# Optimization experiments

Measured on AMD Instinct MI355X. Metric: run time of the kernel, lower is better.

Reference implementation:

```python
import jax, jax.numpy as jnp
import numpy as np

B, N, L = 128, 100, 30
D_FEAT, C, CMD, T = 2112, 512, 512, 4
NEG = -1e30
INV_SQRT_C = np.float32(1.0 / np.sqrt(C))


def setup_inputs() -> dict:
    key = jax.random.key(0)
    ks = iter(jax.random.split(key, 64))

    def lin(out, inn):
        s = 1.0 / np.sqrt(inn)
        W = jax.random.uniform(next(ks), (out, inn), minval=-s, maxval=s, dtype=jnp.float32)
        b = jax.random.uniform(next(ks), (out,), minval=-s, maxval=s, dtype=jnp.float32)
        return W, b

    inp = {}
    inp['images'] = jax.random.normal(next(ks), (B, N, D_FEAT), dtype=jnp.float32)
    inp['q_encoding'] = jax.random.normal(next(ks), (B, CMD), dtype=jnp.float32)
    inp['lstm_outputs'] = jax.random.normal(next(ks), (B, L, CMD), dtype=jnp.float32)
    inp['W_initKB'], inp['b_initKB'] = lin(C, D_FEAT)
    inp['initMem'] = jax.random.normal(next(ks), (1, 1, C), dtype=jnp.float32)
    inp['W_qIn'], inp['b_qIn'] = lin(CMD, CMD)
    Ws, bs = zip(*[lin(CMD, CMD) for _ in range(T)])
    inp['W_qIn2'] = jnp.stack(Ws)
    inp['b_qIn2'] = jnp.stack(bs)
    inp['W_logit'], inp['b_logit'] = lin(1, CMD)
    inp['W_ploc'], inp['b_ploc'] = lin(C, C)
    inp['W_pctx'], inp['b_pctx'] = lin(C, C)
    inp['W_q'], inp['b_q'] = lin(C, 3 * C)
    inp['W_k'], inp['b_k'] = lin(C, 3 * C)
    inp['W_v'], inp['b_v'] = lin(C, 3 * C)
    inp['W_pk'], inp['b_pk'] = lin(C, CMD)
    inp['W_pv'], inp['b_pv'] = lin(C, CMD)
    inp['W_mem'], inp['b_mem'] = lin(C, 2 * C)
    inp['W_comb'], inp['b_comb'] = lin(C, 2 * C)
    inp['q_length'] = jax.random.randint(next(ks), (B,), 1, L + 1)
    inp['entity_num'] = jax.random.randint(next(ks), (B,), 1, N + 1)
    return inp


def _linear(x, W, b):
    return x @ W.T + b


def reference(images, q_encoding, lstm_outputs, W_initKB, b_initKB, initMem,
              W_qIn, b_qIn, W_qIn2, b_qIn2, W_logit, b_logit,
              W_ploc, b_ploc, W_pctx, b_pctx, W_q, b_q, W_k, b_k, W_v, b_v,
              W_pk, b_pk, W_pv, b_pv, W_mem, b_mem, W_comb, b_comb,
              q_length, entity_num):
    # stem (STEM_LINEAR + STEM_NORMALIZE); eval mode so dropouts + var-drop mask are identity
    imgs = images / jnp.maximum(jnp.linalg.norm(images, axis=-1, keepdims=True), 1e-12)
    x_loc = _linear(imgs, W_initKB, b_initKB)                              # [B,N,C]
    x_ctx = jnp.broadcast_to(initMem, x_loc.shape)                         # [B,N,C]
    q_mask = jnp.arange(L)[None, :] < q_length[:, None]                    # apply_mask1d [B,L]
    k_mask = jnp.arange(N)[None, None, :] < entity_num[:, None, None]      # apply_mask2d [B,1,N]
    q_cmd_base = jax.nn.elu(_linear(q_encoding, W_qIn, b_qIn))             # shared qInput layer
    for t in range(T):
        # extract textual command
        q_cmd = _linear(q_cmd_base, W_qIn2[t], b_qIn2[t])                  # [B,CMD]
        raw_att = _linear(q_cmd[:, None, :] * lstm_outputs, W_logit, b_logit)[..., 0]  # [B,L]
        att = jax.nn.softmax(jnp.where(q_mask, raw_att, NEG), axis=-1)
        cmd = jnp.einsum('bl,blc->bc', att, lstm_outputs)                  # [B,CMD]
        # propagate message
        proj_loc = _linear(x_loc, W_ploc, b_ploc)
        proj_ctx = _linear(x_ctx, W_pctx, b_pctx)
        x_joint = jnp.concatenate([x_loc, x_ctx, proj_loc * proj_ctx], axis=-1)  # [B,N,3C]
        queries = _linear(x_joint, W_q, b_q)
        keys = _linear(x_joint, W_k, b_k) * _linear(cmd, W_pk, b_pk)[:, None, :]
        vals = _linear(x_joint, W_v, b_v) * _linear(cmd, W_pv, b_pv)[:, None, :]
        scores = jnp.einsum('bqc,bkc->bqk', queries, keys) * INV_SQRT_C    # [B,N,N]
        prob = jax.nn.softmax(jnp.where(k_mask, scores, NEG), axis=-1)
        message = jnp.einsum('bqk,bkc->bqc', prob, vals)
        x_ctx = _linear(jnp.concatenate([x_ctx, message], axis=-1), W_mem, b_mem)
    return _linear(jnp.concatenate([x_loc, x_ctx], axis=-1), W_comb, b_comb)
```

## Files before the change

kernel.cpp:

```cpp
#include <hip/hip_runtime.h>
#include <math.h>

#define BB 128
#define NN 100
#define LL 30
#define CC 512
#define DFEAT 2112
#define TT 4
#define ROWS (BB * NN)
#define XJLD 1536
#define INV_SQRT_C_F 0.04419417382415922f
#define QH 50
#define VTK 128

typedef __attribute__((ext_vector_type(8))) short short8;
typedef __attribute__((ext_vector_type(4))) float f32x4;

__device__ inline unsigned short f2bf(float f) {
    unsigned u = __float_as_uint(f);
    u += 0x7fff + ((u >> 16) & 1);
    return (unsigned short)(u >> 16);
}
__device__ inline float b2f(unsigned short h) { return __uint_as_float((unsigned)h << 16); }

__device__ inline void async_ld16(const unsigned short* g, unsigned short* l) {
    __builtin_amdgcn_global_load_lds((const __attribute__((address_space(1))) void*)g,
                                     (__attribute__((address_space(3))) void*)l, 16, 0, 0);
}

__global__ __launch_bounds__(256) void rownorm_kernel(const float* __restrict__ img,
                                                      float* __restrict__ inv_norm) {
    int r = blockIdx.x;
    const float* p = img + (size_t)r * DFEAT;
    float s = 0.f;
    for (int i = threadIdx.x; i < DFEAT; i += 256) { float v = p[i]; s += v * v; }
    __shared__ float red[4];
    int lane = threadIdx.x & 63, wid = threadIdx.x >> 6;
#pragma unroll
    for (int off = 32; off > 0; off >>= 1) s += __shfl_down(s, off);
    if (lane == 0) red[wid] = s;
    __syncthreads();
    if (threadIdx.x == 0) {
        float tot = red[0] + red[1] + red[2] + red[3];
        inv_norm[r] = 1.f / fmaxf(sqrtf(tot), 1e-12f);
    }
}

__global__ __launch_bounds__(256) void cvt_kernel(const float* __restrict__ s,
                                                  unsigned short* __restrict__ d, int n4) {
    int i = blockIdx.x * blockDim.x + threadIdx.x;
    if (i < n4) {
        float4 v = ((const float4*)s)[i];
        ushort4 o;
        o.x = f2bf(v.x); o.y = f2bf(v.y); o.z = f2bf(v.z); o.w = f2bf(v.w);
        ((ushort4*)d)[i] = o;
    }
}

__global__ void zero16_kernel(uint4* __restrict__ p, int n) {
    int i = blockIdx.x * blockDim.x + threadIdx.x;
    if (i < n) p[i] = uint4{0u, 0u, 0u, 0u};
}

__global__ void bcast_kernel(const float* __restrict__ m, unsigned short* __restrict__ x) {
    int i = blockIdx.x * blockDim.x + threadIdx.x;
    if (i < ROWS * CC) {
        int r = i >> 9, c = i & (CC - 1);
        x[(size_t)r * XJLD + CC + c] = f2bf(m[c]);
    }
}

template <int MODE, bool AF32, bool OUTF32, bool DUAL, bool VT>
__global__ __launch_bounds__(256) void gemm_mfma(
    const void* __restrict__ A_, int lda,
    const unsigned short* __restrict__ W, int ldw,
    const float* __restrict__ bias,
    void* __restrict__ C_, int ldc,
    void* __restrict__ C2_,
    int K,
    const float* __restrict__ arsc,
    const float* __restrict__ rowscale) {
    __shared__ unsigned short As[128 * 32];
    __shared__ unsigned short Bs[128 * 32];
    const int t = threadIdx.x;
    const int l = t & 63;
    const int wv = t >> 6;
    const int wr = wv >> 1, wc = wv & 1;
    const int lg = l >> 4, lm = l & 15;
    const int m0 = blockIdx.x * 128, n0 = blockIdx.y * 128;

    f32x4 acc[4][4];
#pragma unroll
    for (int mi = 0; mi < 4; ++mi)
#pragma unroll
        for (int ni = 0; ni < 4; ++ni) acc[mi][ni] = {0.f, 0.f, 0.f, 0.f};

    for (int k0 = 0; k0 < K; k0 += 32) {
        if (AF32) {
            const float* Af = (const float*)A_;
            int row = t >> 1, half = t & 1;
            const float* s = Af + (size_t)(m0 + row) * lda + k0 + half * 16;
            float sc = arsc ? arsc[m0 + row] : 1.f;
            float4 v0 = *(const float4*)s, v1 = *(const float4*)(s + 4);
            float4 v2 = *(const float4*)(s + 8), v3 = *(const float4*)(s + 12);
            short8 h0, h1;
            h0[0] = (short)f2bf(v0.x * sc); h0[1] = (short)f2bf(v0.y * sc);
            h0[2] = (short)f2bf(v0.z * sc); h0[3] = (short)f2bf(v0.w * sc);
            h0[4] = (short)f2bf(v1.x * sc); h0[5] = (short)f2bf(v1.y * sc);
            h0[6] = (short)f2bf(v1.z * sc); h0[7] = (short)f2bf(v1.w * sc);
            h1[0] = (short)f2bf(v2.x * sc); h1[1] = (short)f2bf(v2.y * sc);
            h1[2] = (short)f2bf(v2.z * sc); h1[3] = (short)f2bf(v2.w * sc);
            h1[4] = (short)f2bf(v3.x * sc); h1[5] = (short)f2bf(v3.y * sc);
            h1[6] = (short)f2bf(v3.z * sc); h1[7] = (short)f2bf(v3.w * sc);
            *(short8*)&As[row * 32 + half * 16] = h0;
            *(short8*)&As[row * 32 + half * 16 + 8] = h1;
        } else {
            const unsigned short* Ah = (const unsigned short*)A_;
#pragma unroll
            for (int i = 0; i < 2; ++i) {
                int lin = t + i * 256;
                int row = lin >> 2, seg = lin & 3;
                async_ld16(Ah + (size_t)(m0 + row) * lda + k0 + seg * 8, &As[lin * 8]);
            }
        }
#pragma unroll
        for (int i = 0; i < 2; ++i) {
            int lin = t + i * 256;
            int row = lin >> 2, seg = lin & 3;
            async_ld16(W + (size_t)(n0 + row) * ldw + k0 + seg * 8, &Bs[lin * 8]);
        }
        __syncthreads();

        short8 af[4], bq[4];
#pragma unroll
        for (int mi = 0; mi < 4; ++mi)
            af[mi] = *(const short8*)&As[(wr * 64 + mi * 16 + lm) * 32 + lg * 8];
#pragma unroll
        for (int ni = 0; ni < 4; ++ni)
            bq[ni] = *(const short8*)&Bs[(wc * 64 + ni * 16 + lm) * 32 + lg * 8];
#pragma unroll
        for (int mi = 0; mi < 4; ++mi)
#pragma unroll
            for (int ni = 0; ni < 4; ++ni)
                acc[mi][ni] = __builtin_amdgcn_mfma_f32_16x16x32_bf16(af[mi], bq[ni], acc[mi][ni], 0, 0, 0);
        __syncthreads();
    }

#pragma unroll
    for (int mi = 0; mi < 4; ++mi) {
        int rbase = m0 + wr * 64 + mi * 16 + lg * 4;
#pragma unroll
        for (int ni = 0; ni < 4; ++ni) {
            int n = n0 + wc * 64 + ni * 16 + lm;
            float bv = bias[n];
#pragma unroll
            for (int j = 0; j < 4; ++j) {
                int r = rbase + j;
                float v = acc[mi][ni][j] + bv;
                size_t off = (size_t)r * ldc + n;
                if (MODE == 2) v *= b2f(((const unsigned short*)C_)[off]);
                if (MODE == 3) v *= rowscale[(size_t)(r / NN) * CC + n];
                if (OUTF32) {
                    ((float*)C_)[off] = v;
                } else {
                    unsigned short hv = f2bf(v);
                    if (VT) {
                        int b2 = r / NN, rl = r - b2 * NN;
                        ((unsigned short*)C_)[((size_t)b2 * CC + n) * VTK + rl] = hv;
                    } else {
                        ((unsigned short*)C_)[off] = hv;
                        if (DUAL) ((unsigned short*)C2_)[off] = hv;
                    }
                }
            }
        }
    }
}

template <int MODE>
__global__ __launch_bounds__(256) void gemm_small(
    const float* __restrict__ A, const float* __restrict__ W,
    const float* __restrict__ bias, float* __restrict__ C) {
    __shared__ float As[32 * 72];
    __shared__ float Bs[32 * 72];
    const int t = threadIdx.x;
    const int m0 = blockIdx.x * 64, n0 = blockIdx.y * 64;
    const int tr = t >> 4, tc = t & 15;
    float acc[4][4];
#pragma unroll
    for (int i = 0; i < 4; ++i)
#pragma unroll
        for (int j = 0; j < 4; ++j) acc[i][j] = 0.f;

    for (int k0 = 0; k0 < CC; k0 += 32) {
        int row = t >> 2, seg = t & 3;
        {
            const float* s = A + (size_t)(m0 + row) * CC + k0 + seg * 8;
            float4 v0 = *(const float4*)s, v1 = *(const float4*)(s + 4);
            As[(seg * 8 + 0) * 72 + row] = v0.x; As[(seg * 8 + 1) * 72 + row] = v0.y;
            As[(seg * 8 + 2) * 72 + row] = v0.z; As[(seg * 8 + 3) * 72 + row] = v0.w;
            As[(seg * 8 + 4) * 72 + row] = v1.x; As[(seg * 8 + 5) * 72 + row] = v1.y;
            As[(seg * 8 + 6) * 72 + row] = v1.z; As[(seg * 8 + 7) * 72 + row] = v1.w;
        }
        {
            const float* s = W + (size_t)(n0 + row) * CC + k0 + seg * 8;
            float4 v0 = *(const float4*)s, v1 = *(const float4*)(s + 4);
            Bs[(seg * 8 + 0) * 72 + row] = v0.x; Bs[(seg * 8 + 1) * 72 + row] = v0.y;
            Bs[(seg * 8 + 2) * 72 + row] = v0.z; Bs[(seg * 8 + 3) * 72 + row] = v0.w;
            Bs[(seg * 8 + 4) * 72 + row] = v1.x; Bs[(seg * 8 + 5) * 72 + row] = v1.y;
            Bs[(seg * 8 + 6) * 72 + row] = v1.z; Bs[(seg * 8 + 7) * 72 + row] = v1.w;
        }
        __syncthreads();
#pragma unroll
        for (int kk = 0; kk < 32; ++kk) {
            float4 a = *(const float4*)&As[kk * 72 + tr * 4];
            float4 b = *(const float4*)&Bs[kk * 72 + tc * 4];
            float av[4] = {a.x, a.y, a.z, a.w}, bv[4] = {b.x, b.y, b.z, b.w};
#pragma unroll
            for (int i = 0; i < 4; ++i)
#pragma unroll
                for (int j = 0; j < 4; ++j) acc[i][j] = fmaf(av[i], bv[j], acc[i][j]);
        }
        __syncthreads();
    }
#pragma unroll
    for (int i = 0; i < 4; ++i) {
#pragma unroll
        for (int j = 0; j < 4; ++j) {
            int n = n0 + tc * 4 + j;
            float v = acc[i][j] + bias[n];
            if (MODE == 4) v = v > 0.f ? v : expm1f(v);
            C[(size_t)(m0 + tr * 4 + i) * CC + n] = v;
        }
    }
}

__global__ __launch_bounds__(256) void cmd_kernel(
    const float* __restrict__ qcmd, const float* __restrict__ lstm,
    const float* __restrict__ wlogit, const float* __restrict__ blogit,
    const int* __restrict__ qlen, float* __restrict__ cmd) {
    const int b = blockIdx.x;
    const int t = threadIdx.x;
    __shared__ float qw[CC];
    __shared__ float att[LL];
    for (int c = t; c < CC; c += 256) qw[c] = qcmd[b * CC + c] * wlogit[c];
    __syncthreads();
    const int wid = t >> 6, lane = t & 63;
    for (int l = wid; l < LL; l += 4) {
        const float* lp = lstm + ((size_t)b * LL + l) * CC;
        float s = 0.f;
        for (int c = lane; c < CC; c += 64) s = fmaf(qw[c], lp[c], s);
#pragma unroll
        for (int off = 32; off > 0; off >>= 1) s += __shfl_down(s, off);
        if (lane == 0) att[l] = s + blogit[0];
    }
    __syncthreads();
    if (t == 0) {
        int Lq = qlen[b];
        float mx = -1e30f;
        for (int l = 0; l < LL; ++l) {
            if (l >= Lq) att[l] = -1e30f;
            mx = fmaxf(mx, att[l]);
        }
        float sum = 0.f;
        for (int l = 0; l < LL; ++l) { float e = expf(att[l] - mx); att[l] = e; sum += e; }
        float inv = 1.f / sum;
        for (int l = 0; l < LL; ++l) att[l] *= inv;
    }
    __syncthreads();
    for (int c = t; c < CC; c += 256) {
        float s = 0.f;
        for (int l = 0; l < LL; ++l) s = fmaf(att[l], lstm[((size_t)b * LL + l) * CC + c], s);
        cmd[b * CC + c] = s;
    }
}

__global__ __launch_bounds__(256) void attn_mfma_kernel(
    const unsigned short* __restrict__ Qm, const unsigned short* __restrict__ Km,
    const unsigned short* __restrict__ Vt, const int* __restrict__ entnum,
    unsigned short* __restrict__ msg) {
    __shared__ char ldsraw[64 * 132 * 4];
    float* S = (float*)ldsraw;
    unsigned short* Qs = (unsigned short*)ldsraw;
    unsigned short* Ks = (unsigned short*)(ldsraw + 8192);
    const int b = blockIdx.x;
    const int qbase = blockIdx.y * QH;
    const int t = threadIdx.x;
    const int wv = t >> 6, l = t & 63, lg = l >> 4, lm = l & 15;
    const unsigned short* Qp = Qm + ((size_t)b * NN + qbase) * CC;
    const unsigned short* Kp = Km + (size_t)b * NN * CC;

    f32x4 sacc[7];
#pragma unroll
    for (int i = 0; i < 7; ++i) sacc[i] = {0.f, 0.f, 0.f, 0.f};

    for (int k0 = 0; k0 < CC; k0 += 64) {
#pragma unroll
        for (int i = 0; i < 2; ++i) {
            int lin = t + i * 256;
            int row = lin >> 3, seg = lin & 7;
            async_ld16(Qp + (size_t)row * CC + k0 + seg * 8, &Qs[lin * 8]);
        }
#pragma unroll
        for (int i = 0; i < 4; ++i) {
            int lin = t + i * 256;
            if (lin < 896) {
                int row = lin >> 3, seg = lin & 7;
                async_ld16(Kp + (size_t)row * CC + k0 + seg * 8, &Ks[lin * 8]);
            }
        }
        __syncthreads();
#pragma unroll
        for (int kk = 0; kk < 64; kk += 32) {
            short8 a = *(const short8*)&Qs[(wv * 16 + lm) * 64 + kk + lg * 8];
#pragma unroll
            for (int nf = 0; nf < 7; ++nf) {
                short8 bb = *(const short8*)&Ks[(nf * 16 + lm) * 64 + kk + lg * 8];
                sacc[nf] = __builtin_amdgcn_mfma_f32_16x16x32_bf16(a, bb, sacc[nf], 0, 0, 0);
            }
        }
        __syncthreads();
    }
#pragma unroll
    for (int nf = 0; nf < 7; ++nf)
#pragma unroll
        for (int j = 0; j < 4; ++j)
            S[(wv * 16 + lg * 4 + j) * 132 + nf * 16 + lm] = sacc[nf][j] * INV_SQRT_C_F;
    __syncthreads();

    const int en = entnum[b];
    for (int q = wv; q < QH; q += 4) {
        float v0 = (l < en) ? S[q * 132 + l] : -1e30f;
        int k1 = l + 64;
        float v1 = (k1 < en) ? S[q * 132 + k1] : -1e30f;
        float mx = fmaxf(v0, v1);
#pragma unroll
        for (int o = 32; o > 0; o >>= 1) mx = fmaxf(mx, __shfl_xor(mx, o));
        float e0 = (l < en) ? expf(v0 - mx) : 0.f;
        float e1 = (k1 < en) ? expf(v1 - mx) : 0.f;
        float ss = e0 + e1;
#pragma unroll
        for (int o = 32; o > 0; o >>= 1) ss += __shfl_xor(ss, o);
        float inv = 1.f / ss;
        S[q * 132 + l] = e0 * inv;
        S[q * 132 + k1] = e1 * inv;
    }
    __syncthreads();

    f32x4 acc[4][8];
#pragma unroll
    for (int mf = 0; mf < 4; ++mf)
#pragma unroll
        for (int nf = 0; nf < 8; ++nf) acc[mf][nf] = {0.f, 0.f, 0.f, 0.f};

    const unsigned short* Vb = Vt + (size_t)b * CC * VTK;
    for (int ks = 0; ks < 4; ++ks) {
        int k0 = ks * 32;
        short8 pa[4];
#pragma unroll
        for (int mf = 0; mf < 4; ++mf) {
            const float* sp = &S[(mf * 16 + lm) * 132 + k0 + lg * 8];
            short8 h;
#pragma unroll
            for (int jj = 0; jj < 8; ++jj) h[jj] = (short)f2bf(sp[jj]);
            pa[mf] = h;
        }
#pragma unroll
        for (int nf = 0; nf < 8; ++nf) {
            short8 bb = *(const short8*)(Vb + ((size_t)(wv * 128 + nf * 16 + lm)) * VTK + k0 + lg * 8);
#pragma unroll
            for (int mf = 0; mf < 4; ++mf)
                acc[mf][nf] = __builtin_amdgcn_mfma_f32_16x16x32_bf16(pa[mf], bb, acc[mf][nf], 0, 0, 0);
        }
    }
#pragma unroll
    for (int mf = 0; mf < 4; ++mf) {
#pragma unroll
        for (int j = 0; j < 4; ++j) {
            int q = mf * 16 + lg * 4 + j;
            if (q < QH) {
                size_t rb = ((size_t)b * NN + qbase + q) * XJLD;
#pragma unroll
                for (int nf = 0; nf < 8; ++nf)
                    msg[rb + wv * 128 + nf * 16 + lm] = f2bf(acc[mf][nf][j]);
            }
        }
    }
}

extern "C" void kernel_launch(void* const* d_in, const int* in_sizes, int n_in,
                              void* d_out, int out_size, void* d_ws, size_t ws_size,
                              hipStream_t stream) {
    const float* images   = (const float*)d_in[0];
    const float* q_enc    = (const float*)d_in[1];
    const float* lstm     = (const float*)d_in[2];
    const float* W_initKB = (const float*)d_in[3];
    const float* b_initKB = (const float*)d_in[4];
    const float* initMem  = (const float*)d_in[5];
    const float* W_qIn    = (const float*)d_in[6];
    const float* b_qIn    = (const float*)d_in[7];
    const float* W_qIn2   = (const float*)d_in[8];
    const float* b_qIn2   = (const float*)d_in[9];
    const float* W_logit  = (const float*)d_in[10];
    const float* b_logit  = (const float*)d_in[11];
    const float* W_ploc   = (const float*)d_in[12];
    const float* b_ploc   = (const float*)d_in[13];
    const float* W_pctx   = (const float*)d_in[14];
    const float* b_pctx   = (const float*)d_in[15];
    const float* W_q      = (const float*)d_in[16];
    const float* b_q      = (const float*)d_in[17];
    const float* W_k      = (const float*)d_in[18];
    const float* b_k      = (const float*)d_in[19];
    const float* W_v      = (const float*)d_in[20];
    const float* b_v      = (const float*)d_in[21];
    const float* W_pk     = (const float*)d_in[22];
    const float* b_pk     = (const float*)d_in[23];
    const float* W_pv     = (const float*)d_in[24];
    const float* b_pv     = (const float*)d_in[25];
    const float* W_mem    = (const float*)d_in[26];
    const float* b_mem    = (const float*)d_in[27];
    const float* W_comb   = (const float*)d_in[28];
    const float* b_comb   = (const float*)d_in[29];
    const int* q_length   = (const int*)d_in[30];
    const int* entity_num = (const int*)d_in[31];
    (void)in_sizes; (void)n_in; (void)out_size; (void)ws_size;

    char* p = (char*)d_ws;
    auto alloc = [&](size_t bytes) { char* q = p; p += (bytes + 255) & ~(size_t)255; return q; };
    unsigned short* XJ0 = (unsigned short*)alloc((size_t)ROWS * XJLD * 2);
    unsigned short* XJ1 = (unsigned short*)alloc((size_t)ROWS * XJLD * 2);
    unsigned short* Qb  = (unsigned short*)alloc((size_t)ROWS * CC * 2);
    unsigned short* Kb  = (unsigned short*)alloc((size_t)ROWS * CC * 2);
    unsigned short* Vt  = (unsigned short*)alloc((size_t)BB * CC * VTK * 2);
    unsigned short* Wbf = (unsigned short*)alloc((size_t)5013504 * 2);
    float* qcb  = (float*)alloc((size_t)BB * CC * 4);
    float* qcmd = (float*)alloc((size_t)BB * CC * 4);
    float* cmd  = (float*)alloc((size_t)BB * CC * 4);
    float* pk   = (float*)alloc((size_t)BB * CC * 4);
    float* pv   = (float*)alloc((size_t)BB * CC * 4);
    float* invn = (float*)alloc((size_t)ROWS * 4);

    unsigned short* Wi_init = Wbf + 0;
    unsigned short* Wi_ploc = Wbf + 1081344;
    unsigned short* Wi_pctx = Wbf + 1343488;
    unsigned short* Wi_q    = Wbf + 1605632;
    unsigned short* Wi_k    = Wbf + 2392064;
    unsigned short* Wi_v    = Wbf + 3178496;
    unsigned short* Wi_mem  = Wbf + 3964928;
    unsigned short* Wi_comb = Wbf + 4489216;

    auto cvt = [&](const float* src, unsigned short* dst, size_t n) {
        int n4 = (int)(n / 4);
        cvt_kernel<<<dim3((n4 + 255) / 256), dim3(256), 0, stream>>>(src, dst, n4);
    };

    rownorm_kernel<<<dim3(ROWS), dim3(256), 0, stream>>>(images, invn);
    zero16_kernel<<<dim3(((int)((size_t)BB * CC * VTK * 2 / 16) + 255) / 256), dim3(256), 0, stream>>>(
        (uint4*)Vt, (int)((size_t)BB * CC * VTK * 2 / 16));
    cvt(W_initKB, Wi_init, (size_t)CC * DFEAT);
    cvt(W_ploc,  Wi_ploc, (size_t)CC * CC);
    cvt(W_pctx,  Wi_pctx, (size_t)CC * CC);
    cvt(W_q,     Wi_q,    (size_t)CC * 3 * CC);
    cvt(W_k,     Wi_k,    (size_t)CC * 3 * CC);
    cvt(W_v,     Wi_v,    (size_t)CC * 3 * CC);
    cvt(W_mem,   Wi_mem,  (size_t)CC * 2 * CC);
    cvt(W_comb,  Wi_comb, (size_t)CC * 2 * CC);

    dim3 gBig(ROWS / 128, 4), blk(256);
    gemm_mfma<0, true, false, true, false><<<gBig, blk, 0, stream>>>(
        images, DFEAT, Wi_init, DFEAT, b_initKB, XJ0, XJLD, XJ1, DFEAT, invn, nullptr);
    bcast_kernel<<<dim3((ROWS * CC + 255) / 256), dim3(256), 0, stream>>>(initMem, XJ0);
    gemm_small<4><<<dim3(BB / 64, 8), blk, 0, stream>>>(q_enc, W_qIn, b_qIn, qcb);

    for (int t = 0; t < TT; ++t) {
        unsigned short* R  = (t & 1) ? XJ1 : XJ0;
        unsigned short* Wr = (t & 1) ? XJ0 : XJ1;
        gemm_small<0><<<dim3(BB / 64, 8), blk, 0, stream>>>(
            qcb, W_qIn2 + (size_t)t * CC * CC, b_qIn2 + (size_t)t * CC, qcmd);
        cmd_kernel<<<dim3(BB), blk, 0, stream>>>(qcmd, lstm, W_logit, b_logit, q_length, cmd);
        gemm_small<0><<<dim3(BB / 64, 8), blk, 0, stream>>>(cmd, W_pk, b_pk, pk);
        gemm_small<0><<<dim3(BB / 64, 8), blk, 0, stream>>>(cmd, W_pv, b_pv, pv);
        gemm_mfma<0, false, false, false, false><<<gBig, blk, 0, stream>>>(
            R, XJLD, Wi_ploc, CC, b_ploc, R + 2 * CC, XJLD, nullptr, CC, nullptr, nullptr);
        gemm_mfma<2, false, false, false, false><<<gBig, blk, 0, stream>>>(
            R + CC, XJLD, Wi_pctx, CC, b_pctx, R + 2 * CC, XJLD, nullptr, CC, nullptr, nullptr);
        gemm_mfma<0, false, false, false, false><<<gBig, blk, 0, stream>>>(
            R, XJLD, Wi_q, 3 * CC, b_q, Qb, CC, nullptr, 3 * CC, nullptr, nullptr);
        gemm_mfma<3, false, false, false, false><<<gBig, blk, 0, stream>>>(
            R, XJLD, Wi_k, 3 * CC, b_k, Kb, CC, nullptr, 3 * CC, nullptr, pk);
        gemm_mfma<3, false, false, false, true><<<gBig, blk, 0, stream>>>(
            R, XJLD, Wi_v, 3 * CC, b_v, Vt, CC, nullptr, 3 * CC, nullptr, pv);
        attn_mfma_kernel<<<dim3(BB, 2), blk, 0, stream>>>(Qb, Kb, Vt, entity_num, R + 2 * CC);
        gemm_mfma<0, false, false, false, false><<<gBig, blk, 0, stream>>>(
            R + CC, XJLD, Wi_mem, 2 * CC, b_mem, Wr + CC, XJLD, nullptr, 2 * CC, nullptr, nullptr);
    }
    gemm_mfma<0, false, true, false, false><<<gBig, blk, 0, stream>>>(
        XJ0, XJLD, Wi_comb, 2 * CC, b_comb, (float*)d_out, CC, nullptr, 2 * CC, nullptr, nullptr);
}
```

Measured before the change: 1.708 ms.

## Double GEMM K-tile, XOR-swizzle LDS, and remap workgroups across XCDs

The main MFMA GEMM now stages 64-wide K tiles instead of 32, halving the number of barrier pairs per K loop. LDS tiles for the GEMM and the attention score kernel use an XOR swizzle on 16-byte segments to avoid bank conflicts on the strided row reads. The GEMM grid is flattened to 1D and block IDs are remapped so consecutive tiles sharing A rows land on the same XCD for L2 reuse. The cost is double the LDS per block, which may lower occupancy.

Result: faster. 1.575 ms (-7.8%).

```diff
diff --git a/kernel.cpp b/kernel.cpp
--- a/kernel.cpp
+++ b/kernel.cpp
@@ -80,14 +80,18 @@
     int K,
     const float* __restrict__ arsc,
     const float* __restrict__ rowscale) {
-    __shared__ unsigned short As[128 * 32];
-    __shared__ unsigned short Bs[128 * 32];
+    __shared__ unsigned short As[128 * 64];
+    __shared__ unsigned short Bs[128 * 64];
     const int t = threadIdx.x;
     const int l = t & 63;
     const int wv = t >> 6;
     const int wr = wv >> 1, wc = wv & 1;
     const int lg = l >> 4, lm = l & 15;
-    const int m0 = blockIdx.x * 128, n0 = blockIdx.y * 128;
+    const int nwg = gridDim.x;
+    const int qq = nwg >> 3, rr = nwg & 7;
+    const int xcd = blockIdx.x & 7, idx = blockIdx.x >> 3;
+    const int wgid = (xcd < rr ? xcd * (qq + 1) : rr * (qq + 1) + (xcd - rr) * qq) + idx;
+    const int m0 = (wgid >> 2) * 128, n0 = (wgid & 3) * 128;
 
     f32x4 acc[4][4];
 #pragma unroll
@@ -95,54 +99,64 @@
 #pragma unroll
         for (int ni = 0; ni < 4; ++ni) acc[mi][ni] = {0.f, 0.f, 0.f, 0.f};
 
-    for (int k0 = 0; k0 < K; k0 += 32) {
+    for (int k0 = 0; k0 < K; k0 += 64) {
         if (AF32) {
             const float* Af = (const float*)A_;
             int row = t >> 1, half = t & 1;
-            const float* s = Af + (size_t)(m0 + row) * lda + k0 + half * 16;
+            const float* s = Af + (size_t)(m0 + row) * lda + k0 + half * 32;
             float sc = arsc ? arsc[m0 + row] : 1.f;
-            float4 v0 = *(const float4*)s, v1 = *(const float4*)(s + 4);
-            float4 v2 = *(const float4*)(s + 8), v3 = *(const float4*)(s + 12);
-            short8 h0, h1;
-            h0[0] = (short)f2bf(v0.x * sc); h0[1] = (short)f2bf(v0.y * sc);
-            h0[2] = (short)f2bf(v0.z * sc); h0[3] = (short)f2bf(v0.w * sc);
-            h0[4] = (short)f2bf(v1.x * sc); h0[5] = (short)f2bf(v1.y * sc);
-            h0[6] = (short)f2bf(v1.z * sc); h0[7] = (short)f2bf(v1.w * sc);
-            h1[0] = (short)f2bf(v2.x * sc); h1[1] = (short)f2bf(v2.y * sc);
-            h1[2] = (short)f2bf(v2.z * sc); h1[3] = (short)f2bf(v2.w * sc);
-            h1[4] = (short)f2bf(v3.x * sc); h1[5] = (short)f2bf(v3.y * sc);
-            h1[6] = (short)f2bf(v3.z * sc); h1[7] = (short)f2bf(v3.w * sc);
-            *(short8*)&As[row * 32 + half * 16] = h0;
-            *(short8*)&As[row * 32 + half * 16 + 8] = h1;
+#pragma unroll
+            for (int c = 0; c < 4; ++c) {
+                float4 v0 = *(const float4*)(s + c * 8);
+                float4 v1 = *(const float4*)(s + c * 8 + 4);
+                short8 h;
+                h[0] = (short)f2bf(v0.x * sc); h[1] = (short)f2bf(v0.y * sc);
+                h[2] = (short)f2bf(v0.z * sc); h[3] = (short)f2bf(v0.w * sc);
+                h[4] = (short)f2bf(v1.x * sc); h[5] = (short)f2bf(v1.y * sc);
+                h[6] = (short)f2bf(v1.z * sc); h[7] = (short)f2bf(v1.w * sc);
+                int cs = half * 4 + c;
+                *(short8*)&As[row * 64 + ((cs ^ (row & 7)) * 8)] = h;
+            }
         } else {
             const unsigned short* Ah = (const unsigned short*)A_;
 #pragma unroll
-            for (int i = 0; i < 2; ++i) {
+            for (int i = 0; i < 4; ++i) {
                 int lin = t + i * 256;
-                int row = lin >> 2, seg = lin & 3;
-                async_ld16(Ah + (size_t)(m0 + row) * lda + k0 + seg * 8, &As[lin * 8]);
-            }
-        }
-#pragma unroll
-        for (int i = 0; i < 2; ++i) {
+                int row = lin >> 3, seg = lin & 7;
+                async_ld16(Ah + (size_t)(m0 + row) * lda + k0 + ((seg ^ (row & 7)) * 8),
+                           &As[lin * 8]);
+            }
+        }
+#pragma unroll
+        for (int i = 0; i < 4; ++i) {
             int lin = t + i * 256;
-            int row = lin >> 2, seg = lin & 3;
-            async_ld16(W + (size_t)(n0 + row) * ldw + k0 + seg * 8, &Bs[lin * 8]);
+            int row = lin >> 3, seg = lin & 7;
+            async_ld16(W + (size_t)(n0 + row) * ldw + k0 + ((seg ^ (row & 7)) * 8),
+                       &Bs[lin * 8]);
         }
         __syncthreads();
 
-        short8 af[4], bq[4];
-#pragma unroll
-        for (int mi = 0; mi < 4; ++mi)
-            af[mi] = *(const short8*)&As[(wr * 64 + mi * 16 + lm) * 32 + lg * 8];
-#pragma unroll
-        for (int ni = 0; ni < 4; ++ni)
-            bq[ni] = *(const short8*)&Bs[(wc * 64 + ni * 16 + lm) * 32 + lg * 8];
-#pragma unroll
-        for (int mi = 0; mi < 4; ++mi)
-#pragma unroll
-            for (int ni = 0; ni < 4; ++ni)
-                acc[mi][ni] = __builtin_amdgcn_mfma_f32_16x16x32_bf16(af[mi], bq[ni], acc[mi][ni], 0, 0, 0);
+#pragma unroll
+        for (int kk = 0; kk < 2; ++kk) {
+            short8 af[4], bq[4];
+#pragma unroll
+            for (int mi = 0; mi < 4; ++mi) {
+                int row = wr * 64 + mi * 16 + lm;
+                int cs = kk * 4 + lg;
+                af[mi] = *(const short8*)&As[row * 64 + ((cs ^ (row & 7)) * 8)];
+            }
+#pragma unroll
+            for (int ni = 0; ni < 4; ++ni) {
+                int row = wc * 64 + ni * 16 + lm;
+                int cs = kk * 4 + lg;
+                bq[ni] = *(const short8*)&Bs[row * 64 + ((cs ^ (row & 7)) * 8)];
+            }
+#pragma unroll
+            for (int mi = 0; mi < 4; ++mi)
+#pragma unroll
+                for (int ni = 0; ni < 4; ++ni)
+                    acc[mi][ni] = __builtin_amdgcn_mfma_f32_16x16x32_bf16(af[mi], bq[ni], acc[mi][ni], 0, 0, 0);
+        }
         __syncthreads();
     }
 
@@ -299,23 +313,26 @@
         for (int i = 0; i < 2; ++i) {
             int lin = t + i * 256;
             int row = lin >> 3, seg = lin & 7;
-            async_ld16(Qp + (size_t)row * CC + k0 + seg * 8, &Qs[lin * 8]);
+            async_ld16(Qp + (size_t)row * CC + k0 + ((seg ^ (row & 7)) * 8), &Qs[lin * 8]);
         }
 #pragma unroll
         for (int i = 0; i < 4; ++i) {
             int lin = t + i * 256;
             if (lin < 896) {
                 int row = lin >> 3, seg = lin & 7;
-                async_ld16(Kp + (size_t)row * CC + k0 + seg * 8, &Ks[lin * 8]);
+                async_ld16(Kp + (size_t)row * CC + k0 + ((seg ^ (row & 7)) * 8), &Ks[lin * 8]);
             }
         }
         __syncthreads();
 #pragma unroll
-        for (int kk = 0; kk < 64; kk += 32) {
-            short8 a = *(const short8*)&Qs[(wv * 16 + lm) * 64 + kk + lg * 8];
+        for (int kk = 0; kk < 2; ++kk) {
+            int arow = wv * 16 + lm;
+            int cs = kk * 4 + lg;
+            short8 a = *(const short8*)&Qs[arow * 64 + ((cs ^ (arow & 7)) * 8)];
 #pragma unroll
             for (int nf = 0; nf < 7; ++nf) {
-                short8 bb = *(const short8*)&Ks[(nf * 16 + lm) * 64 + kk + lg * 8];
+                int brow = nf * 16 + lm;
+                short8 bb = *(const short8*)&Ks[brow * 64 + ((cs ^ (brow & 7)) * 8)];
                 sacc[nf] = __builtin_amdgcn_mfma_f32_16x16x32_bf16(a, bb, sacc[nf], 0, 0, 0);
             }
         }
@@ -466,7 +483,7 @@
     cvt(W_mem,   Wi_mem,  (size_t)CC * 2 * CC);
     cvt(W_comb,  Wi_comb, (size_t)CC * 2 * CC);
 
-    dim3 gBig(ROWS / 128, 4), blk(256);
+    dim3 gBig((ROWS / 128) * 4), blk(256);
     gemm_mfma<0, true, false, true, false><<<gBig, blk, 0, stream>>>(
         images, DFEAT, Wi_init, DFEAT, b_initKB, XJ0, XJLD, XJ1, DFEAT, invn, nullptr);
     bcast_kernel<<<dim3((ROWS * CC + 255) / 256), dim3(256), 0, stream>>>(initMem, XJ0);
```
